# Kernel tuning notes

Measured on AMD Instinct MI355X. Metric: run time of the kernel, lower is better.

The kernel has to match this reference:

```python
import jax, jax.numpy as jnp
import numpy as np

B, IN_CH, OUT_CH, STYLE_DIM, K, H, W = 16, 512, 512, 512, 3, 32, 32


def setup_inputs() -> dict:
    key = jax.random.key(0)
    k1, k2, k3, k4 = jax.random.split(key, 4)
    return {
        "x": jax.random.normal(k1, (B, IN_CH, H, W), dtype=jnp.float32),
        "style": jax.random.normal(k2, (B, STYLE_DIM), dtype=jnp.float32),
        "aff_weight": jax.random.normal(k3, (IN_CH, STYLE_DIM), dtype=jnp.float32),
        "aff_bias": jnp.zeros((IN_CH,), dtype=jnp.float32),
        "conv_weight": jax.random.normal(k4, (OUT_CH, IN_CH, K, K), dtype=jnp.float32),
    }


def reference(x, style, aff_weight, aff_bias, conv_weight):
    # EqualizedLinearAct with act='linear': y = style @ (W*scale)^T + bias
    style_dim = aff_weight.shape[1]
    aff_scale = 1.0 / np.sqrt(style_dim)  # gain=1.0
    s = style @ (aff_weight * aff_scale).T + aff_bias + 1.0  # [B, in]

    out_ch, in_ch, k, _ = conv_weight.shape
    w_scale = 1.0 / np.sqrt(in_ch * k * k)  # gain / sqrt(in*k*k)
    # per-sample modulated weights: [B, out, in, k, k]
    w = conv_weight[None, :, :, :, :] * s[:, None, :, None, None] * w_scale
    # demodulation
    d = jax.lax.rsqrt(jnp.sum(w * w, axis=(2, 3, 4), keepdims=True) + 1e-8)
    w = w * d

    # groups=B grouped conv == per-sample conv; up=1, flip_weight=True ->
    # plain cross-correlation (same as torch F.conv2d / lax conv default).
    def conv1(xi, wi):
        # xi: [in, H, W], wi: [out, in, k, k]
        return jax.lax.conv_general_dilated(
            xi[None], wi, window_strides=(1, 1), padding="SAME",
            dimension_numbers=("NCHW", "OIHW", "NCHW"))[0]

    return jax.vmap(conv1)(x, w)  # [B, out, H, W]
```

## Files before the change

### kernel.cpp

```cpp
#include <hip/hip_runtime.h>


#define BATCH   16
#define CIN     512
#define COUT    512
#define IMG     32
#define PAD_IMG 34

static constexpr float AFF_SCALE = 0.044194173824159216f;
static constexpr float W_SCALE   = 0.014731391274719739f;

typedef __bf16 bf16x8 __attribute__((ext_vector_type(8)));
typedef float  f32x4  __attribute__((ext_vector_type(4)));

__device__ inline unsigned short f2bf(float f) {
    union { float f; unsigned int u; } v; v.f = f;
    unsigned int u = v.u;
    unsigned int r = (u + 0x7FFFu + ((u >> 16) & 1u)) >> 16;
    return (unsigned short)r;
}

__device__ inline float waveReduceSum(float v) {
    #pragma unroll
    for (int off = 32; off > 0; off >>= 1) v += __shfl_xor(v, off, 64);
    return v;
}

__global__ void compute_s(const float* __restrict__ style,
                          const float* __restrict__ aw,
                          const float* __restrict__ ab,
                          float* __restrict__ s_out) {
    const int i = blockIdx.x * 4 + (threadIdx.x >> 6);
    const int b = blockIdx.y;
    const int lane = threadIdx.x & 63;
    float sum = 0.f;
    #pragma unroll
    for (int k = 0; k < 512; k += 64)
        sum += style[b * 512 + k + lane] * aw[i * 512 + k + lane];
    sum = waveReduceSum(sum);
    if (lane == 0) s_out[b * 512 + i] = sum * AFF_SCALE + ab[i] + 1.0f;
}

__global__ void repack_w(const float* __restrict__ cw,
                         unsigned short* __restrict__ w_t,
                         float* __restrict__ wsq) {
    const int idx = blockIdx.x * 256 + threadIdx.x;
    const float* src = cw + (size_t)idx * 9;
    float acc = 0.f;
    #pragma unroll
    for (int e = 0; e < 9; ++e) {
        float v = src[e];
        acc += v * v;
        w_t[e * (COUT * CIN) + idx] = f2bf(v);
    }
    wsq[idx] = acc;
}

__global__ void compute_scale(const float* __restrict__ s_in,
                              const float* __restrict__ wsq,
                              float* __restrict__ scl) {
    const int o = blockIdx.x * 4 + (threadIdx.x >> 6);
    const int b = blockIdx.y;
    const int lane = threadIdx.x & 63;
    float sum = 0.f;
    #pragma unroll
    for (int i = 0; i < 512; i += 64) {
        float sv = s_in[b * 512 + i + lane];
        sum += sv * sv * wsq[o * 512 + i + lane];
    }
    sum = waveReduceSum(sum);
    if (lane == 0)
        scl[b * 512 + o] = W_SCALE * rsqrtf(W_SCALE * W_SCALE * sum + 1e-8f);
}

__global__ void build_xpad(const float* __restrict__ x,
                           const float* __restrict__ s_in,
                           unsigned short* __restrict__ xpad) {
    const int c0 = blockIdx.x * 64;
    const int hh = blockIdx.y;
    const int b  = blockIdx.z;
    const int tid = threadIdx.x;
    unsigned short* rowbase = xpad + (((size_t)b * PAD_IMG + hh) * PAD_IMG) * 512;

    if (hh == 0 || hh == PAD_IMG - 1) {
        for (int j = tid; j < 34 * 32; j += 256) {
            int ww = j >> 5, cp = (j & 31) * 2;
            *(unsigned int*)(rowbase + (size_t)ww * 512 + c0 + cp) = 0u;
        }
        return;
    }

    __shared__ float t[64][33];
    const int h = hh - 1;
    {
        const int wx = tid & 31;
        const int cb = (tid >> 5) * 8;
        const float* xb = x + (((size_t)b * 512 + c0 + cb) * IMG + h) * IMG + wx;
        #pragma unroll
        for (int j = 0; j < 8; ++j)
            t[cb + j][wx] = xb[(size_t)j * (IMG * IMG)] * s_in[b * 512 + c0 + cb + j];
    }
    __syncthreads();
    {
        const int p  = tid >> 3;
        const int cc = (tid & 7) * 8;
        unsigned short* dst = rowbase + (size_t)(p + 1) * 512 + c0 + cc;
        uint4 pk;
        pk.x = (unsigned)f2bf(t[cc + 0][p]) | ((unsigned)f2bf(t[cc + 1][p]) << 16);
        pk.y = (unsigned)f2bf(t[cc + 2][p]) | ((unsigned)f2bf(t[cc + 3][p]) << 16);
        pk.z = (unsigned)f2bf(t[cc + 4][p]) | ((unsigned)f2bf(t[cc + 5][p]) << 16);
        pk.w = (unsigned)f2bf(t[cc + 6][p]) | ((unsigned)f2bf(t[cc + 7][p]) << 16);
        *(uint4*)dst = pk;
    }
    if (tid < 64) {
        int ww = (tid >> 5) ? (PAD_IMG - 1) : 0;
        int cp = (tid & 31) * 2;
        *(unsigned int*)(rowbase + (size_t)ww * 512 + c0 + cp) = 0u;
    }
}

__global__ __launch_bounds__(256, 2) void conv_mfma(
    const unsigned short* __restrict__ wt,
    const unsigned short* __restrict__ xpad,
    const float* __restrict__ scl,
    float* __restrict__ out)
{
    __shared__ unsigned short Alds[128 * 32];
    __shared__ unsigned short Blds[128 * 32];
    __shared__ float sclds[128];

    const int tid = threadIdx.x;
    const int b   = blockIdx.z;
    const int m0  = blockIdx.x * 128;
    const int h0  = blockIdx.y * 4;

    if (tid < 128) sclds[tid] = scl[b * 512 + m0 + tid];

    const int wid  = tid >> 6;
    const int lane = tid & 63;
    const int wm = wid & 1, wn = wid >> 1;

    const f32x4 vzero = {0.f, 0.f, 0.f, 0.f};
    f32x4 acc[4][4];
    #pragma unroll
    for (int i = 0; i < 4; ++i)
        #pragma unroll
        for (int j = 0; j < 4; ++j) acc[i][j] = vzero;

    int aOff[2], bOff[2], ldsBase[2];
    #pragma unroll
    for (int r = 0; r < 2; ++r) {
        int f   = r * 256 + tid;
        int row = f >> 2;
        int col = (f & 3) * 8;
        aOff[r] = row * 512 + col;
        bOff[r] = ((row >> 5) * PAD_IMG + (row & 31)) * 512 + col;
        ldsBase[r] = (r * 256 + wid * 64) * 8;
    }

    const int arow = (wm * 64 + (lane & 15)) * 32 + (lane >> 4) * 8;
    const int brow = (wn * 64 + (lane & 15)) * 32 + (lane >> 4) * 8;

    for (int e = 0; e < 9; ++e) {
        const int kh = e / 3, kw = e % 3;
        const unsigned short* Abase = wt + (size_t)e * (COUT * CIN) + (size_t)m0 * 512;
        const unsigned short* Bbase =
            xpad + (((size_t)b * PAD_IMG + h0 + kh) * PAD_IMG + kw) * 512;
        for (int kc = 0; kc < 512; kc += 32) {
            __syncthreads();
            #pragma unroll
            for (int r = 0; r < 2; ++r)
                __builtin_amdgcn_global_load_lds(
                    (const __attribute__((address_space(1))) void*)(Abase + aOff[r] + kc),
                    (__attribute__((address_space(3))) void*)(&Alds[ldsBase[r]]),
                    16, 0, 0);
            #pragma unroll
            for (int r = 0; r < 2; ++r)
                __builtin_amdgcn_global_load_lds(
                    (const __attribute__((address_space(1))) void*)(Bbase + bOff[r] + kc),
                    (__attribute__((address_space(3))) void*)(&Blds[ldsBase[r]]),
                    16, 0, 0);
            __syncthreads();

            bf16x8 af[4], bfr[4];
            #pragma unroll
            for (int mi = 0; mi < 4; ++mi)
                af[mi] = *(const bf16x8*)(&Alds[arow + mi * 16 * 32]);
            #pragma unroll
            for (int ni = 0; ni < 4; ++ni)
                bfr[ni] = *(const bf16x8*)(&Blds[brow + ni * 16 * 32]);
            #pragma unroll
            for (int mi = 0; mi < 4; ++mi)
                #pragma unroll
                for (int ni = 0; ni < 4; ++ni)
                    acc[mi][ni] = __builtin_amdgcn_mfma_f32_16x16x32_bf16(
                        af[mi], bfr[ni], acc[mi][ni], 0, 0, 0);
        }
    }

    const int colp = lane & 15;
    const int rowq = (lane >> 4) * 4;
    const int p0 = h0 * 32;
    #pragma unroll
    for (int mi = 0; mi < 4; ++mi) {
        #pragma unroll
        for (int ni = 0; ni < 4; ++ni) {
            const int p = p0 + wn * 64 + ni * 16 + colp;
            #pragma unroll
            for (int r2 = 0; r2 < 4; ++r2) {
                const int ol = wm * 64 + mi * 16 + rowq + r2;
                out[(((size_t)b * 512 + m0 + ol) << 10) + p] =
                    acc[mi][ni][r2] * sclds[ol];
            }
        }
    }
}

extern "C" void kernel_launch(void* const* d_in, const int* in_sizes, int n_in,
                              void* d_out, int out_size, void* d_ws, size_t ws_size,
                              hipStream_t stream) {
    const float* x     = (const float*)d_in[0];
    const float* style = (const float*)d_in[1];
    const float* aw    = (const float*)d_in[2];
    const float* ab    = (const float*)d_in[3];
    const float* cw    = (const float*)d_in[4];
    float* out = (float*)d_out;

    char* ws = (char*)d_ws;
    float* s_buf          = (float*)(ws);
    float* scl            = (float*)(ws + 32768);
    float* wsq            = (float*)(ws + 65536);
    unsigned short* w_t   = (unsigned short*)(ws + 1114112);
    unsigned short* x_pad = (unsigned short*)(ws + 5832704);

    compute_s<<<dim3(128, 16), 256, 0, stream>>>(style, aw, ab, s_buf);
    repack_w<<<dim3(1024), 256, 0, stream>>>(cw, w_t, wsq);
    compute_scale<<<dim3(128, 16), 256, 0, stream>>>(s_buf, wsq, scl);
    build_xpad<<<dim3(8, 34, 16), 256, 0, stream>>>(x, s_buf, x_pad);
    conv_mfma<<<dim3(4, 8, 16), 256, 0, stream>>>(w_t, x_pad, scl, out);
}
```

Baseline: 203.1 us.

## Merge prep kernels, fold demod scale into conv, swizzle LDS layout

```diff
diff --git a/kernel.cpp b/kernel.cpp
--- a/kernel.cpp
+++ b/kernel.cpp
@@ -26,51 +26,46 @@
     return v;
 }
 
-__global__ void compute_s(const float* __restrict__ style,
-                          const float* __restrict__ aw,
-                          const float* __restrict__ ab,
-                          float* __restrict__ s_out) {
-    const int i = blockIdx.x * 4 + (threadIdx.x >> 6);
-    const int b = blockIdx.y;
-    const int lane = threadIdx.x & 63;
-    float sum = 0.f;
-    #pragma unroll
-    for (int k = 0; k < 512; k += 64)
-        sum += style[b * 512 + k + lane] * aw[i * 512 + k + lane];
-    sum = waveReduceSum(sum);
-    if (lane == 0) s_out[b * 512 + i] = sum * AFF_SCALE + ab[i] + 1.0f;
-}
-
-__global__ void repack_w(const float* __restrict__ cw,
-                         unsigned short* __restrict__ w_t,
-                         float* __restrict__ wsq) {
-    const int idx = blockIdx.x * 256 + threadIdx.x;
-    const float* src = cw + (size_t)idx * 9;
-    float acc = 0.f;
-    #pragma unroll
-    for (int e = 0; e < 9; ++e) {
-        float v = src[e];
-        acc += v * v;
-        w_t[e * (COUT * CIN) + idx] = f2bf(v);
-    }
-    wsq[idx] = acc;
-}
-
-__global__ void compute_scale(const float* __restrict__ s_in,
-                              const float* __restrict__ wsq,
-                              float* __restrict__ scl) {
-    const int o = blockIdx.x * 4 + (threadIdx.x >> 6);
-    const int b = blockIdx.y;
-    const int lane = threadIdx.x & 63;
-    float sum = 0.f;
-    #pragma unroll
-    for (int i = 0; i < 512; i += 64) {
-        float sv = s_in[b * 512 + i + lane];
-        sum += sv * sv * wsq[o * 512 + i + lane];
-    }
-    sum = waveReduceSum(sum);
-    if (lane == 0)
-        scl[b * 512 + o] = W_SCALE * rsqrtf(W_SCALE * W_SCALE * sum + 1e-8f);
+__global__ void prep1(const float* __restrict__ cw,
+                      const float* __restrict__ style,
+                      const float* __restrict__ aw,
+                      const float* __restrict__ ab,
+                      unsigned short* __restrict__ w_t,
+                      float* __restrict__ wsq,
+                      float* __restrict__ s_out,
+                      float* __restrict__ ssq_out) {
+    const int tid = threadIdx.x;
+    if (blockIdx.x < 1024) {
+        __shared__ float wl[2304];
+        const float* src = cw + (size_t)blockIdx.x * 2304;
+        for (int j = tid; j < 2304; j += 256) wl[j] = src[j];
+        __syncthreads();
+        const int idx = blockIdx.x * 256 + tid;
+        const int base = tid * 9;
+        float acc = 0.f;
+        #pragma unroll
+        for (int e = 0; e < 9; ++e) {
+            float v = wl[base + e];
+            acc += v * v;
+            w_t[e * (COUT * CIN) + idx] = f2bf(v);
+        }
+        wsq[idx] = acc;
+    } else {
+        const int q = blockIdx.x - 1024;
+        const int b = q >> 7;
+        const int i = (q & 127) * 4 + (tid >> 6);
+        const int lane = tid & 63;
+        float sum = 0.f;
+        #pragma unroll
+        for (int k = 0; k < 512; k += 64)
+            sum += style[b * 512 + k + lane] * aw[i * 512 + k + lane];
+        sum = waveReduceSum(sum);
+        if (lane == 0) {
+            float s = sum * AFF_SCALE + ab[i] + 1.0f;
+            s_out[b * 512 + i] = s;
+            ssq_out[b * 512 + i] = s * s;
+        }
+    }
 }
 
 __global__ void build_xpad(const float* __restrict__ x,
@@ -122,7 +117,8 @@
 __global__ __launch_bounds__(256, 2) void conv_mfma(
     const unsigned short* __restrict__ wt,
     const unsigned short* __restrict__ xpad,
-    const float* __restrict__ scl,
+    const float* __restrict__ wsq,
+    const float* __restrict__ ssq,
     float* __restrict__ out)
 {
     __shared__ unsigned short Alds[128 * 32];
@@ -134,7 +130,21 @@
     const int m0  = blockIdx.x * 128;
     const int h0  = blockIdx.y * 4;
 
-    if (tid < 128) sclds[tid] = scl[b * 512 + m0 + tid];
+    {
+        const int ol   = tid >> 1;
+        const int half = tid & 1;
+        const f32x4* w4 = (const f32x4*)(wsq + (size_t)(m0 + ol) * 512 + half * 256);
+        const f32x4* s4 = (const f32x4*)(ssq + b * 512 + half * 256);
+        float sum = 0.f;
+        #pragma unroll 4
+        for (int i = 0; i < 64; ++i) {
+            f32x4 a = w4[i], c = s4[i];
+            sum += a.x * c.x + a.y * c.y + a.z * c.z + a.w * c.w;
+        }
+        sum += __shfl_xor(sum, 1, 64);
+        if (half == 0)
+            sclds[ol] = W_SCALE * rsqrtf(W_SCALE * W_SCALE * sum + 1e-8f);
+    }
 
     const int wid  = tid >> 6;
     const int lane = tid & 63;
@@ -152,14 +162,18 @@
     for (int r = 0; r < 2; ++r) {
         int f   = r * 256 + tid;
         int row = f >> 2;
-        int col = (f & 3) * 8;
-        aOff[r] = row * 512 + col;
-        bOff[r] = ((row >> 5) * PAD_IMG + (row & 31)) * 512 + col;
+        int pos = f & 3;
+        int c   = pos ^ ((row >> 1) & 3);
+        aOff[r] = row * 512 + c * 8;
+        bOff[r] = ((row >> 5) * PAD_IMG + (row & 31)) * 512 + c * 8;
         ldsBase[r] = (r * 256 + wid * 64) * 8;
     }
 
-    const int arow = (wm * 64 + (lane & 15)) * 32 + (lane >> 4) * 8;
-    const int brow = (wn * 64 + (lane & 15)) * 32 + (lane >> 4) * 8;
+    const int rl   = lane & 15;
+    const int kch  = lane >> 4;
+    const int swz  = (kch ^ ((rl >> 1) & 3)) * 8;
+    const int arow = (wm * 64 + rl) * 32 + swz;
+    const int brow = (wn * 64 + rl) * 32 + swz;
 
     for (int e = 0; e < 9; ++e) {
         const int kh = e / 3, kw = e % 3;
@@ -228,14 +242,12 @@
 
     char* ws = (char*)d_ws;
     float* s_buf          = (float*)(ws);
-    float* scl            = (float*)(ws + 32768);
+    float* ssq            = (float*)(ws + 32768);
     float* wsq            = (float*)(ws + 65536);
     unsigned short* w_t   = (unsigned short*)(ws + 1114112);
     unsigned short* x_pad = (unsigned short*)(ws + 5832704);
 
-    compute_s<<<dim3(128, 16), 256, 0, stream>>>(style, aw, ab, s_buf);
-    repack_w<<<dim3(1024), 256, 0, stream>>>(cw, w_t, wsq);
-    compute_scale<<<dim3(128, 16), 256, 0, stream>>>(s_buf, wsq, scl);
+    prep1<<<dim3(3072), 256, 0, stream>>>(cw, style, aw, ab, w_t, wsq, s_buf, ssq);
     build_xpad<<<dim3(8, 34, 16), 256, 0, stream>>>(x, s_buf, x_pad);
-    conv_mfma<<<dim3(4, 8, 16), 256, 0, stream>>>(w_t, x_pad, scl, out);
-}
+    conv_mfma<<<dim3(4, 8, 16), 256, 0, stream>>>(w_t, x_pad, wsq, ssq, out);
+}
```

New measurement: 216.5 us. 6.6% more time.
